# Kernel tuning notes

Measured on AMD Instinct MI355X. Metric: run time of the kernel, lower is better.

## Reference

```python
import jax, jax.numpy as jnp
import numpy as np

N_NODES, N_EDGES, WIDTH = 50000, 640000, 128


def setup_inputs() -> dict:
    key = jax.random.key(0)
    k1, k2, k3 = jax.random.split(key, 3)
    x = jax.random.normal(k1, (N_NODES, WIDTH), dtype=jnp.float32)
    e = jax.random.randint(k2, (2, N_EDGES), 0, N_NODES, dtype=jnp.int32)
    # LinearBlock(2*width, width): Linear(256 -> 128) + ReLU
    W = jax.random.normal(k3, (WIDTH, 2 * WIDTH), dtype=jnp.float32) * (1.0 / np.sqrt(2 * WIDTH))
    b = jnp.zeros((WIDTH,), dtype=jnp.float32)
    return {"x": x, "e": e, "W": W, "b": b}


def reference(x, e, W, b):
    src, dst = e[0], e[1]
    # gather-subtract: diffs[k] = x[dst_k] - x[src_k]  -> [E, width]
    diffs = x[dst] - x[src]
    n = x.shape[0]
    # scatter_max over destination nodes; torch_scatter leaves empty segments at 0
    maxes = jax.ops.segment_max(diffs, dst, num_segments=n)  # [N, width]
    deg = jax.ops.segment_sum(jnp.ones((dst.shape[0],), jnp.float32), dst, num_segments=n)
    maxes = jnp.where((deg > 0)[:, None], maxes, 0.0)
    # LinearBlock (Linear + ReLU) on concat, then residual
    h = jnp.concatenate([x, maxes], axis=1)  # [N, 2*width]
    return x + jax.nn.relu(h @ W.T + b)
```

## Files before the change

### kernel.cpp

```cpp
#include <hip/hip_runtime.h>
#include <hip/hip_bf16.h>

#define WIDTH   128
#define NNODES  50000
#define NEDGES  640000
#define NTILES  3125
#define TILES_PER_BLOCK 8
#define WLDS_STRIDE 264
#define CAP     64

typedef __attribute__((ext_vector_type(8))) short  short8;
typedef __attribute__((ext_vector_type(4))) short  short4_t;
typedef __attribute__((ext_vector_type(4))) float  float4_t;

__device__ inline short f2bf(float f) {
    union { float f; unsigned int u; } a;
    a.f = f;
    unsigned int r = a.u + 0x7FFFu + ((a.u >> 16) & 1u);
    return (short)(r >> 16);
}

__global__ __launch_bounds__(256) void fill_kernel(
    const int* __restrict__ e, int* __restrict__ counts, int* __restrict__ buckets)
{
    int i = blockIdx.x * 256 + threadIdx.x;
    if (i >= NEDGES) return;
    int src = e[i];
    int dst = e[NEDGES + i];
    int pos = atomicAdd(&counts[dst], 1);
    if (pos < CAP) buckets[dst * CAP + pos] = src;
}

__global__ __launch_bounds__(256) void gather_min_kernel(
    const float* __restrict__ x, const int* __restrict__ counts,
    const int* __restrict__ buckets, unsigned int* __restrict__ maxes_u32)
{
    int wave = (blockIdx.x * 256 + threadIdx.x) >> 6;
    int lane = threadIdx.x & 63;
    if (wave >= NNODES) return;
    int node = wave;
    int deg  = counts[node];
    deg = deg > CAP ? CAP : deg;

    int myidx = (lane < deg) ? buckets[node * CAP + lane] : 0;

    int c = lane * 2;
    float2 m; m.x = 3.4e38f; m.y = 3.4e38f;
#pragma unroll 1
    for (int j0 = 0; j0 < deg; j0 += 8) {
        float2 v[8];
#pragma unroll
        for (int u = 0; u < 8; ++u) {
            int jc = j0 + u;
            jc = jc < deg ? jc : deg - 1;
            int src = __shfl(myidx, jc);
            v[u] = *(const float2*)(x + (size_t)src * WIDTH + c);
        }
#pragma unroll
        for (int u = 0; u < 8; ++u) {
            m.x = fminf(m.x, v[u].x);
            m.y = fminf(m.y, v[u].y);
        }
    }

    float2 o;
    if (deg > 0) {
        float2 xv = *(const float2*)(x + (size_t)node * WIDTH + c);
        o.x = xv.x - m.x;
        o.y = xv.y - m.y;
    } else {
        o.x = 0.f; o.y = 0.f;
    }
    unsigned int lo = (unsigned short)f2bf(o.x);
    unsigned int hi = (unsigned short)f2bf(o.y);
    maxes_u32[(size_t)node * 64 + lane] = lo | (hi << 16);
}

__global__ __launch_bounds__(256, 2) void fused_gemm_kernel(
    const float* __restrict__ x, const short* __restrict__ maxes,
    const float* __restrict__ W, const float* __restrict__ b,
    float* __restrict__ out)
{
    __shared__ short Wlds[WIDTH * WLDS_STRIDE];

    const int t = threadIdx.x;

#pragma unroll
    for (int i = 0; i < 32; ++i) {
        int idx4 = t + i * 256;
        int flat = idx4 << 2;
        float4 w = *(const float4*)(W + flat);
        int n = flat >> 8;
        int k = flat & 255;
        short4_t s;
        s.x = f2bf(w.x); s.y = f2bf(w.y); s.z = f2bf(w.z); s.w = f2bf(w.w);
        *(short4_t*)&Wlds[n * WLDS_STRIDE + k] = s;
    }
    __syncthreads();

    const int wave  = t >> 6;
    const int lane  = t & 63;
    const int lm    = lane & 15;
    const int quad  = lane >> 4;
    const int nhalf = wave & 1;
    const int wpair = wave >> 1;
    const int ncol_base = nhalf * 64;

    short8 bfrag[4][8];
#pragma unroll
    for (int nt = 0; nt < 4; ++nt) {
        int n = ncol_base + nt * 16 + lm;
#pragma unroll
        for (int kt = 0; kt < 8; ++kt) {
            int k = kt * 32 + quad * 8;
            bfrag[nt][kt] = *(const short8*)&Wlds[n * WLDS_STRIDE + k];
        }
    }

    const int tile0 = blockIdx.x * TILES_PER_BLOCK;
#pragma unroll 1
    for (int i = 0; i < 4; ++i) {
        int tile = tile0 + 2 * i + wpair;
        if (tile >= NTILES) break;
        int row = tile * 16 + lm;
        const float* xr = x     + (size_t)row * WIDTH;
        const short* mr = maxes + (size_t)row * WIDTH;

        float4_t acc[4];
#pragma unroll
        for (int nt = 0; nt < 4; ++nt) { acc[nt].x = 0.f; acc[nt].y = 0.f; acc[nt].z = 0.f; acc[nt].w = 0.f; }

#pragma unroll
        for (int kt = 0; kt < 8; ++kt) {
            int k = kt * 32 + quad * 8;
            short8 afrag;
            if (k < WIDTH) {
                float4 v0 = *(const float4*)(xr + k);
                float4 v1 = *(const float4*)(xr + k + 4);
                afrag[0] = f2bf(v0.x); afrag[1] = f2bf(v0.y);
                afrag[2] = f2bf(v0.z); afrag[3] = f2bf(v0.w);
                afrag[4] = f2bf(v1.x); afrag[5] = f2bf(v1.y);
                afrag[6] = f2bf(v1.z); afrag[7] = f2bf(v1.w);
            } else {
                afrag = *(const short8*)(mr + (k - WIDTH));
            }
#pragma unroll
            for (int nt = 0; nt < 4; ++nt) {
                acc[nt] = __builtin_amdgcn_mfma_f32_16x16x32_bf16(
                    afrag, bfrag[nt][kt], acc[nt], 0, 0, 0);
            }
        }

#pragma unroll
        for (int nt = 0; nt < 4; ++nt) {
            int col = ncol_base + nt * 16 + lm;
            float bias = b[col];
#pragma unroll
            for (int r = 0; r < 4; ++r) {
                int orow = tile * 16 + quad * 4 + r;
                float v = acc[nt][r] + bias;
                v = v > 0.f ? v : 0.f;
                size_t off = (size_t)orow * WIDTH + col;
                out[off] = x[off] + v;
            }
        }
    }
}

extern "C" void kernel_launch(void* const* d_in, const int* in_sizes, int n_in,
                              void* d_out, int out_size, void* d_ws, size_t ws_size,
                              hipStream_t stream) {
    const float* x = (const float*)d_in[0];
    const int*   e = (const int*)  d_in[1];
    const float* W = (const float*)d_in[2];
    const float* b = (const float*)d_in[3];
    float* out = (float*)d_out;

    int*          counts  = (int*)d_ws;
    int*          buckets = (int*)d_ws + 65536;
    unsigned int* maxes   = (unsigned int*)((int*)d_ws + 65536 + NNODES * CAP);

    hipMemsetAsync(counts, 0, 65536 * sizeof(int), stream);

    fill_kernel<<<(NEDGES + 255) / 256, 256, 0, stream>>>(e, counts, buckets);

    gather_min_kernel<<<(NNODES + 3) / 4, 256, 0, stream>>>(x, counts, buckets, maxes);

    int gemm_blocks = (NTILES + TILES_PER_BLOCK - 1) / TILES_PER_BLOCK;
    fused_gemm_kernel<<<gemm_blocks, 256, 0, stream>>>(x, (const short*)maxes, W, b, out);
}
```

Measured before the change: 173.0 us.

## Pre-convert x to bf16 for half-width gathers and GEMM A-operand loads

Adds a kernel that converts x to a bf16 copy in workspace and zeroes the degree counters in the same pass, which removes the separate memset. The gather-min kernel then reads bf16 rows with two neighbors per wave pass, halving gather bytes, and the GEMM loads bf16 x directly instead of converting fp32 on the fly. GEMM tiles per block drop from 8 to 4 for more blocks. The min is now taken over bf16-rounded values, which changes rounding slightly, and the fp32 fallback runs only when the workspace is too small.

```diff
diff --git a/kernel.cpp b/kernel.cpp
--- a/kernel.cpp
+++ b/kernel.cpp
@@ -5,7 +5,7 @@
 #define NNODES  50000
 #define NEDGES  640000
 #define NTILES  3125
-#define TILES_PER_BLOCK 8
+#define TILES_PER_BLOCK 4
 #define WLDS_STRIDE 264
 #define CAP     64
 
@@ -18,6 +18,25 @@
     a.f = f;
     unsigned int r = a.u + 0x7FFFu + ((a.u >> 16) & 1u);
     return (short)(r >> 16);
+}
+__device__ inline unsigned int pack2bf(float a, float b) {
+    unsigned int lo = (unsigned short)f2bf(a);
+    unsigned int hi = (unsigned short)f2bf(b);
+    return lo | (hi << 16);
+}
+__device__ inline float bflo(unsigned int u) { return __uint_as_float(u << 16); }
+__device__ inline float bfhi(unsigned int u) { return __uint_as_float(u & 0xFFFF0000u); }
+
+__global__ __launch_bounds__(256) void convert_zero_kernel(
+    const float* __restrict__ x, uint2* __restrict__ xb2, int* __restrict__ counts)
+{
+    int i = blockIdx.x * 256 + threadIdx.x;
+    float4 v = *(const float4*)(x + (size_t)i * 4);
+    uint2 p;
+    p.x = pack2bf(v.x, v.y);
+    p.y = pack2bf(v.z, v.w);
+    xb2[i] = p;
+    if (i < 16384) *(int4*)(counts + i * 4) = make_int4(0, 0, 0, 0);
 }
 
 __global__ __launch_bounds__(256) void fill_kernel(
@@ -31,9 +50,9 @@
     if (pos < CAP) buckets[dst * CAP + pos] = src;
 }
 
-__global__ __launch_bounds__(256) void gather_min_kernel(
-    const float* __restrict__ x, const int* __restrict__ counts,
-    const int* __restrict__ buckets, unsigned int* __restrict__ maxes_u32)
+__global__ __launch_bounds__(256) void gather_min_bf16_kernel(
+    const uint2* __restrict__ xb2, const int* __restrict__ counts,
+    const int* __restrict__ buckets, uint2* __restrict__ maxes2)
 {
     int wave = (blockIdx.x * 256 + threadIdx.x) >> 6;
     int lane = threadIdx.x & 63;
@@ -43,7 +62,58 @@
     deg = deg > CAP ? CAP : deg;
 
     int myidx = (lane < deg) ? buckets[node * CAP + lane] : 0;
-
+    int h  = lane >> 5;
+    int cl = lane & 31;
+
+    float4 m; m.x = 3.4e38f; m.y = 3.4e38f; m.z = 3.4e38f; m.w = 3.4e38f;
+#pragma unroll 1
+    for (int j0 = 0; j0 < deg; j0 += 16) {
+        uint2 v[8];
+#pragma unroll
+        for (int u = 0; u < 8; ++u) {
+            int jc = j0 + 2 * u + h;
+            jc = jc < deg ? jc : deg - 1;
+            int src = __shfl(myidx, jc);
+            v[u] = xb2[(size_t)src * 32 + cl];
+        }
+#pragma unroll
+        for (int u = 0; u < 8; ++u) {
+            m.x = fminf(m.x, bflo(v[u].x));
+            m.y = fminf(m.y, bfhi(v[u].x));
+            m.z = fminf(m.z, bflo(v[u].y));
+            m.w = fminf(m.w, bfhi(v[u].y));
+        }
+    }
+    m.x = fminf(m.x, __shfl_xor(m.x, 32));
+    m.y = fminf(m.y, __shfl_xor(m.y, 32));
+    m.z = fminf(m.z, __shfl_xor(m.z, 32));
+    m.w = fminf(m.w, __shfl_xor(m.w, 32));
+
+    if (h == 0) {
+        uint2 o;
+        if (deg > 0) {
+            uint2 xv = xb2[(size_t)node * 32 + cl];
+            o.x = pack2bf(bflo(xv.x) - m.x, bfhi(xv.x) - m.y);
+            o.y = pack2bf(bflo(xv.y) - m.z, bfhi(xv.y) - m.w);
+        } else {
+            o.x = 0u; o.y = 0u;
+        }
+        maxes2[(size_t)node * 32 + cl] = o;
+    }
+}
+
+__global__ __launch_bounds__(256) void gather_min_fp32_kernel(
+    const float* __restrict__ x, const int* __restrict__ counts,
+    const int* __restrict__ buckets, unsigned int* __restrict__ maxes_u32)
+{
+    int wave = (blockIdx.x * 256 + threadIdx.x) >> 6;
+    int lane = threadIdx.x & 63;
+    if (wave >= NNODES) return;
+    int node = wave;
+    int deg  = counts[node];
+    deg = deg > CAP ? CAP : deg;
+
+    int myidx = (lane < deg) ? buckets[node * CAP + lane] : 0;
     int c = lane * 2;
     float2 m; m.x = 3.4e38f; m.y = 3.4e38f;
 #pragma unroll 1
@@ -62,22 +132,19 @@
             m.y = fminf(m.y, v[u].y);
         }
     }
-
     float2 o;
     if (deg > 0) {
         float2 xv = *(const float2*)(x + (size_t)node * WIDTH + c);
         o.x = xv.x - m.x;
         o.y = xv.y - m.y;
-    } else {
-        o.x = 0.f; o.y = 0.f;
-    }
-    unsigned int lo = (unsigned short)f2bf(o.x);
-    unsigned int hi = (unsigned short)f2bf(o.y);
-    maxes_u32[(size_t)node * 64 + lane] = lo | (hi << 16);
-}
-
+    } else { o.x = 0.f; o.y = 0.f; }
+    maxes_u32[(size_t)node * 64 + lane] = pack2bf(o.x, o.y);
+}
+
+template<bool XB>
 __global__ __launch_bounds__(256, 2) void fused_gemm_kernel(
-    const float* __restrict__ x, const short* __restrict__ maxes,
+    const float* __restrict__ x, const short* __restrict__ xb,
+    const short* __restrict__ maxes,
     const float* __restrict__ W, const float* __restrict__ b,
     float* __restrict__ out)
 {
@@ -119,12 +186,13 @@
 
     const int tile0 = blockIdx.x * TILES_PER_BLOCK;
 #pragma unroll 1
-    for (int i = 0; i < 4; ++i) {
+    for (int i = 0; i < TILES_PER_BLOCK / 2; ++i) {
         int tile = tile0 + 2 * i + wpair;
         if (tile >= NTILES) break;
         int row = tile * 16 + lm;
-        const float* xr = x     + (size_t)row * WIDTH;
-        const short* mr = maxes + (size_t)row * WIDTH;
+        const float* xr  = x     + (size_t)row * WIDTH;
+        const short* xbr = XB ? (xb + (size_t)row * WIDTH) : nullptr;
+        const short* mr  = maxes + (size_t)row * WIDTH;
 
         float4_t acc[4];
 #pragma unroll
@@ -135,12 +203,16 @@
             int k = kt * 32 + quad * 8;
             short8 afrag;
             if (k < WIDTH) {
-                float4 v0 = *(const float4*)(xr + k);
-                float4 v1 = *(const float4*)(xr + k + 4);
-                afrag[0] = f2bf(v0.x); afrag[1] = f2bf(v0.y);
-                afrag[2] = f2bf(v0.z); afrag[3] = f2bf(v0.w);
-                afrag[4] = f2bf(v1.x); afrag[5] = f2bf(v1.y);
-                afrag[6] = f2bf(v1.z); afrag[7] = f2bf(v1.w);
+                if (XB) {
+                    afrag = *(const short8*)(xbr + k);
+                } else {
+                    float4 v0 = *(const float4*)(xr + k);
+                    float4 v1 = *(const float4*)(xr + k + 4);
+                    afrag[0] = f2bf(v0.x); afrag[1] = f2bf(v0.y);
+                    afrag[2] = f2bf(v0.z); afrag[3] = f2bf(v0.w);
+                    afrag[4] = f2bf(v1.x); afrag[5] = f2bf(v1.y);
+                    afrag[6] = f2bf(v1.z); afrag[7] = f2bf(v1.w);
+                }
             } else {
                 afrag = *(const short8*)(mr + (k - WIDTH));
             }
@@ -176,16 +248,30 @@
     const float* b = (const float*)d_in[3];
     float* out = (float*)d_out;
 
-    int*          counts  = (int*)d_ws;
-    int*          buckets = (int*)d_ws + 65536;
-    unsigned int* maxes   = (unsigned int*)((int*)d_ws + 65536 + NNODES * CAP);
-
-    hipMemsetAsync(counts, 0, 65536 * sizeof(int), stream);
-
-    fill_kernel<<<(NEDGES + 255) / 256, 256, 0, stream>>>(e, counts, buckets);
-
-    gather_min_kernel<<<(NNODES + 3) / 4, 256, 0, stream>>>(x, counts, buckets, maxes);
+    char* ws = (char*)d_ws;
+    int*          counts  = (int*)ws;
+    int*          buckets = (int*)(ws + 262144);
+    unsigned int* maxes   = (unsigned int*)(ws + 262144 + 12800000);
+    short*        xb      = (short*)(ws + 262144 + 2 * 12800000);
+
+    const size_t need_xb = 262144 + 3ull * 12800000;
+    const bool use_xb = (ws_size >= need_xb);
 
     int gemm_blocks = (NTILES + TILES_PER_BLOCK - 1) / TILES_PER_BLOCK;
-    fused_gemm_kernel<<<gemm_blocks, 256, 0, stream>>>(x, (const short*)maxes, W, b, out);
-}
+
+    if (use_xb) {
+        convert_zero_kernel<<<6250, 256, 0, stream>>>(x, (uint2*)xb, counts);
+        fill_kernel<<<(NEDGES + 255) / 256, 256, 0, stream>>>(e, counts, buckets);
+        gather_min_bf16_kernel<<<(NNODES + 3) / 4, 256, 0, stream>>>(
+            (const uint2*)xb, counts, buckets, (uint2*)maxes);
+        fused_gemm_kernel<true><<<gemm_blocks, 256, 0, stream>>>(
+            x, xb, (const short*)maxes, W, b, out);
+    } else {
+        hipMemsetAsync(counts, 0, 262144, stream);
+        fill_kernel<<<(NEDGES + 255) / 256, 256, 0, stream>>>(e, counts, buckets);
+        gather_min_fp32_kernel<<<(NNODES + 3) / 4, 256, 0, stream>>>(
+            x, counts, buckets, maxes);
+        fused_gemm_kernel<false><<<gemm_blocks, 256, 0, stream>>>(
+            x, nullptr, (const short*)maxes, W, b, out);
+    }
+}
```

Result: faster. 161.2 us (-6.8%).
